# Kernel tuning notes

Measured on AMD Instinct MI355X. Metric: run time of the kernel, lower is better.

## Reference

```python
import jax, jax.numpy as jnp
import numpy as np

VX, VY = 0.16, 0.16
X_OFFSET = VX / 2 + 0.0      # vx/2 + offset[0]
Y_OFFSET = VY / 2 + (-39.68) # vy/2 + offset[1]
BN_EPS = 1e-5
V, P, C_IN, C_OUT = 40000, 32, 4, 64


def setup_inputs() -> dict:
    key = jax.random.key(0)
    k0, k1, k2, k3 = jax.random.split(key, 4)
    voxels = jax.random.normal(k0, (V, P, C_IN), dtype=jnp.float32)
    num_point_per_voxel = jnp.maximum(
        jax.random.randint(k1, (V,), 0, P + 1), 1).astype(jnp.int32)
    coors = jax.random.randint(k2, (V, 2), 0, 400).astype(jnp.int32)
    W = jax.random.normal(k3, (C_OUT, C_IN + 5), dtype=jnp.float32) * 0.1
    gamma = jnp.ones((C_OUT,), dtype=jnp.float32)
    beta = jnp.zeros((C_OUT,), dtype=jnp.float32)
    return {"voxels": voxels, "num_point_per_voxel": num_point_per_voxel,
            "coors": coors, "W": W, "gamma": gamma, "beta": beta}


def reference(voxels, num_point_per_voxel, coors, W, gamma, beta):
    npts = num_point_per_voxel.astype(voxels.dtype)  # [V]
    xyz = voxels[:, :, :3]
    # cluster offset: subtract per-pillar mean of valid points
    points_mean = jnp.sum(xyz, axis=1, keepdims=True) / npts[:, None, None]
    f_cluster = xyz - points_mean  # [V, P, 3]
    # pillar-center offset
    cx = coors[:, 0].astype(voxels.dtype) * VX + X_OFFSET  # [V]
    cy = coors[:, 1].astype(voxels.dtype) * VY + Y_OFFSET
    f_center = jnp.stack([voxels[:, :, 0] - cx[:, None],
                          voxels[:, :, 1] - cy[:, None]], axis=-1)  # [V, P, 2]
    features = jnp.concatenate([voxels, f_cluster, f_center], axis=-1)  # [V, P, 9]
    # zero out padded points
    point_ids = jnp.arange(P, dtype=jnp.int32)[None, :]
    mask = (num_point_per_voxel[:, None] > point_ids).astype(features.dtype)
    features = features * mask[:, :, None]
    # 1x1 conv == per-point linear: [V, P, 9] x [64, 9] -> [V, P, 64]
    x = jnp.einsum('vpc,oc->vpo', features, W)
    # BatchNorm1d (train mode): stats over (voxel, point) dims per channel
    mean = jnp.mean(x, axis=(0, 1))
    var = jnp.var(x, axis=(0, 1))
    x = (x - mean) * jax.lax.rsqrt(var + BN_EPS) * gamma + beta
    x = jax.nn.relu(x)
    # max over points -> [V, 64]
    return jnp.max(x, axis=1)
```

## Files before the change

kernel.cpp:

```cpp
#include <hip/hip_runtime.h>
#include <hip/hip_bf16.h>

#define V_N   40000
#define P_N   32
#define NTOT  (V_N * P_N)
#define VXc   0.16f
#define VYc   0.16f
#define XOFF  0.08f
#define YOFF  (-39.6f)
#define BN_EPS 1e-5f

#define SBLK  625
#define PBLK  2500

#define FOR_S(X) X(0) X(1) X(2) X(3) X(4) X(5) X(6) X(7) X(8)
#define FOR_M(X) \
  X(0,0) X(0,1) X(0,2) X(0,3) X(0,4) X(0,5) X(0,6) X(0,7) X(0,8) \
  X(1,1) X(1,2) X(1,3) X(1,4) X(1,5) X(1,6) X(1,7) X(1,8) \
  X(2,2) X(2,3) X(2,4) X(2,5) X(2,6) X(2,7) X(2,8) \
  X(3,3) X(3,4) X(3,5) X(3,6) X(3,7) X(3,8) \
  X(4,4) X(4,5) X(4,6) X(4,7) X(4,8) \
  X(5,5) X(5,6) X(5,7) X(5,8) \
  X(6,6) X(6,7) X(6,8) \
  X(7,7) X(7,8) \
  X(8,8)

__device__ __forceinline__ float wave_sum(float x) {
#pragma unroll
    for (int m = 1; m < 64; m <<= 1) x += __shfl_xor(x, m, 64);
    return x;
}

__global__ __launch_bounds__(256) void stats_kernel(
    const float4* __restrict__ voxels,
    const int*    __restrict__ npts_arr,
    const int*    __restrict__ coors,
    float*        __restrict__ stats)
{
    const int lane = threadIdx.x & 63;
    const int p    = lane & 31;
    const int half = lane >> 5;
    const int gw   = (blockIdx.x * 256 + threadIdx.x) >> 6;
    const int nw   = (SBLK * 256) >> 6;

#define DECL_S(i)   float S##i = 0.f;
#define DECL_M(i,j) float M##i##_##j = 0.f;
    FOR_S(DECL_S)
    FOR_M(DECL_M)

    for (int vb = gw * 2; vb < V_N; vb += nw * 2) {
        const int v = vb + half;
        float4 q = voxels[(size_t)v * P_N + p];

        float sx = q.x, sy = q.y, sz = q.z;
#pragma unroll
        for (int m = 1; m < 32; m <<= 1) {
            sx += __shfl_xor(sx, m, 64);
            sy += __shfl_xor(sy, m, 64);
            sz += __shfl_xor(sz, m, 64);
        }
        const int   npts = npts_arr[v];
        const float inv  = 1.f / (float)npts;
        const float cx = (float)coors[2 * v]     * VXc + XOFF;
        const float cy = (float)coors[2 * v + 1] * VYc + YOFF;

        const float g  = (p < npts) ? 1.f : 0.f;
        const float f0 = q.x * g;
        const float f1 = q.y * g;
        const float f2 = q.z * g;
        const float f3 = q.w * g;
        const float f4 = (q.x - sx * inv) * g;
        const float f5 = (q.y - sy * inv) * g;
        const float f6 = (q.z - sz * inv) * g;
        const float f7 = (q.x - cx) * g;
        const float f8 = (q.y - cy) * g;

#define ACC_S(i)   S##i += f##i;
#define ACC_M(i,j) M##i##_##j = fmaf(f##i, f##j, M##i##_##j);
        FOR_S(ACC_S)
        FOR_M(ACC_M)
    }

#define RED_S(i)   S##i = wave_sum(S##i);
#define RED_M(i,j) M##i##_##j = wave_sum(M##i##_##j);
    FOR_S(RED_S)
    FOR_M(RED_M)

    __shared__ float red[4][54];
    const int wib = threadIdx.x >> 6;
    if (lane == 0) {
        float* r = red[wib];
        int k = 0;
#define ST_S(i)   r[k++] = S##i;
#define ST_M(i,j) r[k++] = M##i##_##j;
        FOR_S(ST_S)
        FOR_M(ST_M)
    }
    __syncthreads();
    if (threadIdx.x < 54) {
        float s = red[0][threadIdx.x] + red[1][threadIdx.x]
                + red[2][threadIdx.x] + red[3][threadIdx.x];
        atomicAdd(&stats[threadIdx.x], s);
    }
}

__global__ __launch_bounds__(256) void pfn_kernel(
    const float4* __restrict__ voxels,
    const int*    __restrict__ npts_arr,
    const int*    __restrict__ coors,
    const float*  __restrict__ W,
    const float*  __restrict__ gamma,
    const float*  __restrict__ beta,
    const float*  __restrict__ stats,
    float*        __restrict__ out)
{
    __shared__ float4 sq[4][P_N];
    const int wib  = threadIdx.x >> 6;
    const int lane = threadIdx.x & 63;
    const int pl   = lane & 31;

    float w[9];
#pragma unroll
    for (int c = 0; c < 9; ++c) w[c] = W[lane * 9 + c];

    const float invN = 1.f / (float)NTOT;
    float mean = 0.f;
#pragma unroll
    for (int c = 0; c < 9; ++c) mean = fmaf(w[c], stats[c], mean);
    mean *= invN;

    float ex2 = 0.f;
    {
        int k = 9;
#pragma unroll
        for (int i = 0; i < 9; ++i)
#pragma unroll
            for (int j = i; j < 9; ++j) {
                const float coef = (i == j) ? 1.f : 2.f;
                ex2 = fmaf(coef * w[i] * w[j], stats[k], ex2);
                ++k;
            }
    }
    ex2 *= invN;
    const float var   = ex2 - mean * mean;
    const float scale = gamma[lane] * rsqrtf(var + BN_EPS);
    const float bias  = fmaf(-mean, scale, beta[lane]);

    const float a0 = (w[0] + w[4] + w[7]) * scale;
    const float a1 = (w[1] + w[5] + w[8]) * scale;
    const float a2 = (w[2] + w[6]) * scale;
    const float a3 =  w[3] * scale;
    const float u4 = w[4] * scale, u5 = w[5] * scale, u6 = w[6] * scale;
    const float u7 = w[7] * scale, u8 = w[8] * scale;

    const int gw = (blockIdx.x * 256 + threadIdx.x) >> 6;

#pragma unroll
    for (int it = 0; it < 4; ++it) {
        const int v = gw * 4 + it;

        float4 q = voxels[(size_t)v * P_N + pl];
        float sx = q.x, sy = q.y, sz = q.z;
#pragma unroll
        for (int m = 1; m < 32; m <<= 1) {
            sx += __shfl_xor(sx, m, 64);
            sy += __shfl_xor(sy, m, 64);
            sz += __shfl_xor(sz, m, 64);
        }
        if (lane < 32) sq[wib][lane] = q;
        __builtin_amdgcn_wave_barrier();

        const int   npts = npts_arr[v];
        const float inv  = 1.f / (float)npts;
        const float mx = sx * inv, my = sy * inv, mz = sz * inv;
        const float cx = (float)coors[2 * v]     * VXc + XOFF;
        const float cy = (float)coors[2 * v + 1] * VYc + YOFF;
        const float b  = -(mx * u4 + my * u5 + mz * u6 + cx * u7 + cy * u8);

        float macc = -3.4e38f;
#pragma unroll
        for (int p = 0; p < P_N; ++p) {
            float4 t = sq[wib][p];
            float d = fmaf(t.x, a0, fmaf(t.y, a1, fmaf(t.z, a2, t.w * a3)));
            macc = (p < npts) ? fmaxf(macc, d) : macc;
        }
        float mfin = macc + b;
        if (npts < P_N) mfin = fmaxf(mfin, 0.f);
        out[(size_t)v * 64 + lane] = fmaxf(mfin + bias, 0.f);
        __builtin_amdgcn_wave_barrier();
    }
}

extern "C" void kernel_launch(void* const* d_in, const int* in_sizes, int n_in,
                              void* d_out, int out_size, void* d_ws, size_t ws_size,
                              hipStream_t stream)
{
    const float4* voxels = (const float4*)d_in[0];
    const int*    npts   = (const int*)d_in[1];
    const int*    coors  = (const int*)d_in[2];
    const float*  W      = (const float*)d_in[3];
    const float*  gamma  = (const float*)d_in[4];
    const float*  beta   = (const float*)d_in[5];
    float*        out    = (float*)d_out;
    float*        stats  = (float*)d_ws;

    hipMemsetAsync(stats, 0, 54 * sizeof(float), stream);
    stats_kernel<<<SBLK, 256, 0, stream>>>(voxels, npts, coors, stats);
    pfn_kernel<<<PBLK, 256, 0, stream>>>(voxels, npts, coors, W, gamma, beta,
                                         stats, out);
}
```

Before: 125.7 us.

## Cache pillar means from stats pass and use readlane loops bounded by npts

The stats kernel now writes each pillar's xyz mean to workspace, so the second kernel no longer repeats the shuffle reduction. The PFN kernel handles two voxels per wave load and broadcasts point features with readlane instead of staging them in LDS, looping only over valid points. The stats grid size is doubled and the atomic accumulators are padded to separate cache lines to cut contention. The costs are scalar-serialized readlane loops with data-dependent trip counts and an extra global write and read of the means.

```diff
diff --git a/kernel.cpp b/kernel.cpp
--- a/kernel.cpp
+++ b/kernel.cpp
@@ -10,8 +10,9 @@
 #define YOFF  (-39.6f)
 #define BN_EPS 1e-5f
 
-#define SBLK  625
+#define SBLK  1250
 #define PBLK  2500
+#define CSTR  32
 
 #define FOR_S(X) X(0) X(1) X(2) X(3) X(4) X(5) X(6) X(7) X(8)
 #define FOR_M(X) \
@@ -31,11 +32,16 @@
     return x;
 }
 
+__device__ __forceinline__ float rdlane(float x, int l) {
+    return __uint_as_float(__builtin_amdgcn_readlane(__float_as_uint(x), l));
+}
+
 __global__ __launch_bounds__(256) void stats_kernel(
     const float4* __restrict__ voxels,
     const int*    __restrict__ npts_arr,
     const int*    __restrict__ coors,
-    float*        __restrict__ stats)
+    float*        __restrict__ stats,
+    float4*       __restrict__ means)
 {
     const int lane = threadIdx.x & 63;
     const int p    = lane & 31;
@@ -61,17 +67,20 @@
         }
         const int   npts = npts_arr[v];
         const float inv  = 1.f / (float)npts;
+        const float mx = sx * inv, my = sy * inv, mz = sz * inv;
         const float cx = (float)coors[2 * v]     * VXc + XOFF;
         const float cy = (float)coors[2 * v + 1] * VYc + YOFF;
+
+        if (p == 0) means[v] = make_float4(mx, my, mz, 0.f);
 
         const float g  = (p < npts) ? 1.f : 0.f;
         const float f0 = q.x * g;
         const float f1 = q.y * g;
         const float f2 = q.z * g;
         const float f3 = q.w * g;
-        const float f4 = (q.x - sx * inv) * g;
-        const float f5 = (q.y - sy * inv) * g;
-        const float f6 = (q.z - sz * inv) * g;
+        const float f4 = (q.x - mx) * g;
+        const float f5 = (q.y - my) * g;
+        const float f6 = (q.z - mz) * g;
         const float f7 = (q.x - cx) * g;
         const float f8 = (q.y - cy) * g;
 
@@ -100,7 +109,7 @@
     if (threadIdx.x < 54) {
         float s = red[0][threadIdx.x] + red[1][threadIdx.x]
                 + red[2][threadIdx.x] + red[3][threadIdx.x];
-        atomicAdd(&stats[threadIdx.x], s);
+        atomicAdd(&stats[threadIdx.x * CSTR], s);
     }
 }
 
@@ -112,12 +121,11 @@
     const float*  __restrict__ gamma,
     const float*  __restrict__ beta,
     const float*  __restrict__ stats,
+    const float4* __restrict__ means,
     float*        __restrict__ out)
 {
-    __shared__ float4 sq[4][P_N];
+    const int lane = threadIdx.x & 63;
     const int wib  = threadIdx.x >> 6;
-    const int lane = threadIdx.x & 63;
-    const int pl   = lane & 31;
 
     float w[9];
 #pragma unroll
@@ -126,7 +134,7 @@
     const float invN = 1.f / (float)NTOT;
     float mean = 0.f;
 #pragma unroll
-    for (int c = 0; c < 9; ++c) mean = fmaf(w[c], stats[c], mean);
+    for (int c = 0; c < 9; ++c) mean = fmaf(w[c], stats[c * CSTR], mean);
     mean *= invN;
 
     float ex2 = 0.f;
@@ -137,7 +145,7 @@
 #pragma unroll
             for (int j = i; j < 9; ++j) {
                 const float coef = (i == j) ? 1.f : 2.f;
-                ex2 = fmaf(coef * w[i] * w[j], stats[k], ex2);
+                ex2 = fmaf(coef * w[i] * w[j], stats[k * CSTR], ex2);
                 ++k;
             }
     }
@@ -153,41 +161,59 @@
     const float u4 = w[4] * scale, u5 = w[5] * scale, u6 = w[6] * scale;
     const float u7 = w[7] * scale, u8 = w[8] * scale;
 
-    const int gw = (blockIdx.x * 256 + threadIdx.x) >> 6;
-
-#pragma unroll
-    for (int it = 0; it < 4; ++it) {
-        const int v = gw * 4 + it;
-
-        float4 q = voxels[(size_t)v * P_N + pl];
-        float sx = q.x, sy = q.y, sz = q.z;
-#pragma unroll
-        for (int m = 1; m < 32; m <<= 1) {
-            sx += __shfl_xor(sx, m, 64);
-            sy += __shfl_xor(sy, m, 64);
-            sz += __shfl_xor(sz, m, 64);
+    const int gwave = blockIdx.x * 4 + wib;
+
+#pragma unroll
+    for (int it = 0; it < 2; ++it) {
+        const int vA = gwave * 4 + it * 2;
+        const int vB = vA + 1;
+
+        const int vv = vA + (lane >> 5);
+        const float4 q = voxels[(size_t)vv * P_N + (lane & 31)];
+
+        const int nA = __builtin_amdgcn_readfirstlane(npts_arr[vA]);
+        const int nB = __builtin_amdgcn_readfirstlane(npts_arr[vB]);
+
+        const float4 mA = means[vA];
+        const float4 mB = means[vB];
+        const float cxA = (float)coors[2 * vA]     * VXc + XOFF;
+        const float cyA = (float)coors[2 * vA + 1] * VYc + YOFF;
+        const float cxB = (float)coors[2 * vB]     * VXc + XOFF;
+        const float cyB = (float)coors[2 * vB + 1] * VYc + YOFF;
+
+        const float bA = -fmaf(mA.x, u4, fmaf(mA.y, u5, fmaf(mA.z, u6,
+                           fmaf(cxA, u7, cyA * u8))));
+        const float bB = -fmaf(mB.x, u4, fmaf(mB.y, u5, fmaf(mB.z, u6,
+                           fmaf(cxB, u7, cyB * u8))));
+
+        float maxA = -3.4e38f;
+#pragma unroll 4
+        for (int p = 0; p < nA; ++p) {
+            const float tx = rdlane(q.x, p);
+            const float ty = rdlane(q.y, p);
+            const float tz = rdlane(q.z, p);
+            const float tw = rdlane(q.w, p);
+            const float d  = fmaf(tx, a0, fmaf(ty, a1, fmaf(tz, a2, tw * a3)));
+            maxA = fmaxf(maxA, d);
         }
-        if (lane < 32) sq[wib][lane] = q;
-        __builtin_amdgcn_wave_barrier();
-
-        const int   npts = npts_arr[v];
-        const float inv  = 1.f / (float)npts;
-        const float mx = sx * inv, my = sy * inv, mz = sz * inv;
-        const float cx = (float)coors[2 * v]     * VXc + XOFF;
-        const float cy = (float)coors[2 * v + 1] * VYc + YOFF;
-        const float b  = -(mx * u4 + my * u5 + mz * u6 + cx * u7 + cy * u8);
-
-        float macc = -3.4e38f;
-#pragma unroll
-        for (int p = 0; p < P_N; ++p) {
-            float4 t = sq[wib][p];
-            float d = fmaf(t.x, a0, fmaf(t.y, a1, fmaf(t.z, a2, t.w * a3)));
-            macc = (p < npts) ? fmaxf(macc, d) : macc;
+        float maxB = -3.4e38f;
+#pragma unroll 4
+        for (int p = 0; p < nB; ++p) {
+            const float tx = rdlane(q.x, p + 32);
+            const float ty = rdlane(q.y, p + 32);
+            const float tz = rdlane(q.z, p + 32);
+            const float tw = rdlane(q.w, p + 32);
+            const float d  = fmaf(tx, a0, fmaf(ty, a1, fmaf(tz, a2, tw * a3)));
+            maxB = fmaxf(maxB, d);
         }
-        float mfin = macc + b;
-        if (npts < P_N) mfin = fmaxf(mfin, 0.f);
-        out[(size_t)v * 64 + lane] = fmaxf(mfin + bias, 0.f);
-        __builtin_amdgcn_wave_barrier();
+
+        float mfA = maxA + bA;
+        if (nA < P_N) mfA = fmaxf(mfA, 0.f);
+        out[(size_t)vA * 64 + lane] = fmaxf(mfA + bias, 0.f);
+
+        float mfB = maxB + bB;
+        if (nB < P_N) mfB = fmaxf(mfB, 0.f);
+        out[(size_t)vB * 64 + lane] = fmaxf(mfB + bias, 0.f);
     }
 }
 
@@ -202,10 +228,12 @@
     const float*  gamma  = (const float*)d_in[4];
     const float*  beta   = (const float*)d_in[5];
     float*        out    = (float*)d_out;
-    float*        stats  = (float*)d_ws;
-
-    hipMemsetAsync(stats, 0, 54 * sizeof(float), stream);
-    stats_kernel<<<SBLK, 256, 0, stream>>>(voxels, npts, coors, stats);
+
+    float*  stats = (float*)d_ws;
+    float4* means = (float4*)((char*)d_ws + 8192);
+
+    hipMemsetAsync(stats, 0, 54 * CSTR * sizeof(float), stream);
+    stats_kernel<<<SBLK, 256, 0, stream>>>(voxels, npts, coors, stats, means);
     pfn_kernel<<<PBLK, 256, 0, stream>>>(voxels, npts, coors, W, gamma, beta,
-                                         stats, out);
-}
+                                         stats, means, out);
+}
```

Result: no change. 127.0 us (+1.0%).
